# Optimization experiments

Hardware: AMD Instinct MI355X
Metric: run time of the kernel (lower is better)

The kernel has to match this reference:

```python
import jax, jax.numpy as jnp
import numpy as np

IN_SIZE = 224
KERNEL = 5
STRIDE = 1
IN_CH = 16
OUT_CH = 64
LAMB = 5.0
LR = 0.005
GAMMA = 0.99
EPS_ = 0.01
NH = (IN_SIZE - KERNEL) // STRIDE + 1          # 220 output positions per side
NB_TILES = NH * NH                              # 48400 tiles


def setup_inputs() -> dict:
    key = jax.random.key(0)
    k1, k2 = jax.random.split(key)
    x = jax.random.normal(k1, (1, IN_CH, IN_SIZE, IN_SIZE), dtype=jnp.float32)
    # torch.nn.init.uniform_(param, a=0, b=1)
    W = jax.random.uniform(k2, (OUT_CH, IN_CH, KERNEL, KERNEL), dtype=jnp.float32)
    exp_avg = jnp.zeros((OUT_CH,), dtype=jnp.float32)
    return {"x": x, "W": W, "exp_avg": exp_avg, "clamped": 0}


def _inhibition(out):
    out = jax.nn.relu(out)
    m = jnp.max(out, axis=1, keepdims=True)     # max over channel dim
    out = out / (m + 1e-9)
    return out ** LAMB


def _flatten_input(x):
    # mirrors x.unfold(2,k,s).unfold(3,k,s) -> [T, C*k*k] with (C, kh, kw) ordering
    starts = jnp.arange(NH) * STRIDE
    rows = starts[:, None] + jnp.arange(KERNEL)  # [NH, K]
    p = x[0][:, rows]                            # [C, NH, K, W]
    p = p[:, :, :, rows]                         # [C, NH, K, NH, K]
    p = p.transpose(1, 3, 0, 2, 4)               # [NH, NH, C, K, K]
    return p.reshape(NB_TILES, -1)               # [T, D]


def reference(x, W, exp_avg, clamped):
    # forward conv + inhibition
    out = jax.lax.conv_general_dilated(
        x, W, (STRIDE, STRIDE), 'VALID',
        dimension_numbers=('NCHW', 'OIHW', 'NCHW'))
    out = _inhibition(out)                       # [1, O, NH, NH]

    # Hebbian FullyOrthogonal update (no-grad buffer update in the original)
    y = out[0].transpose(1, 2, 0).reshape(-1, OUT_CH)   # [T, O]
    xf = _flatten_input(x)                               # [T, D]
    Wf = W.reshape(OUT_CH, -1)                           # [O, D]
    # mean_t( lr * (y_t (x) x_t - y_t (x) (y_t W)) ) = lr/T * (Y^T X - (Y^T Y) W)
    yty = y.T @ y                                        # [O, O]
    avg_delta = (LR / NB_TILES) * (y.T @ xf - yty @ Wf)  # [O, D]
    Wnew = jax.nn.relu(Wf + avg_delta).reshape(OUT_CH, IN_CH, KERNEL, KERNEL)
    exp_new = GAMMA * exp_avg + (1.0 - GAMMA) * jnp.mean(y, axis=0)

    # weight decay scaling
    A = exp_new / jnp.mean(exp_new)
    gfp = EPS_ * jnp.tanh(-EPS_ * (A - 1.0)) + 1.0
    gfn = 1.0 / gfp
    pos = jnp.where(Wnew > 0, Wnew, 0.0) * gfp.reshape(-1, 1, 1, 1)
    neg = jnp.where(Wnew < 0, Wnew, 0.0) * gfn.reshape(-1, 1, 1, 1)
    Wfinal = pos + neg
    return out, Wfinal, exp_new
```

## Files before the change

kernel.cpp:

```cpp
#include <hip/hip_runtime.h>
#include <stdint.h>

#define IN_SIZE 224
#define KER 5
#define IN_CH 16
#define OUT_CH 64
#define NH 220
#define NB_TILES (NH * NH)
#define XCH (IN_SIZE * IN_SIZE)
#define OUT_PLANE NB_TILES
#define KP2 51200
#define XS 52224
#define XTROWS 50304
#define LR_OVER_NB ((float)(0.005 / 48400.0))
#define GAMMA_F 0.99f
#define ONE_MINUS_GAMMA 0.01f
#define EPS_F 0.01f

#define NCHUNK 64
#define CK 800
#define PSTRIDE (64 * 512)
#define BROW 24

typedef __attribute__((ext_vector_type(8))) short short8;
typedef __attribute__((ext_vector_type(4))) float floatx4;

__device__ inline uint16_t f2bf(float f) {
    uint32_t u = __float_as_uint(f);
    return (uint16_t)((u + 0x7FFFu + ((u >> 16) & 1u)) >> 16);
}
__device__ inline float bf2f(uint16_t h) { return __uint_as_float((uint32_t)h << 16); }

__global__ __launch_bounds__(256) void prepa_kernel(const float* __restrict__ x,
                                                    uint16_t* __restrict__ xth,
                                                    uint16_t* __restrict__ xtl,
                                                    const float* __restrict__ W,
                                                    uint16_t* __restrict__ wrh,
                                                    uint16_t* __restrict__ wrl) {
    int blk = blockIdx.x;
    if (blk < 197) {
        int addr = blk * 256 + threadIdx.x;
        if (addr >= XTROWS) return;
        uint32_t dh[8], dl[8];
        if (addr < XCH) {
#pragma unroll
            for (int q = 0; q < 8; q++) {
                float v0 = x[(2 * q) * XCH + addr];
                float v1 = x[(2 * q + 1) * XCH + addr];
                uint16_t h0 = f2bf(v0), h1 = f2bf(v1);
                uint16_t l0 = f2bf(v0 - bf2f(h0)), l1 = f2bf(v1 - bf2f(h1));
                dh[q] = (uint32_t)h0 | ((uint32_t)h1 << 16);
                dl[q] = (uint32_t)l0 | ((uint32_t)l1 << 16);
            }
        } else {
#pragma unroll
            for (int q = 0; q < 8; q++) { dh[q] = 0u; dl[q] = 0u; }
        }
        *(uint4*)(xth + addr * 16) = make_uint4(dh[0], dh[1], dh[2], dh[3]);
        *(uint4*)(xth + addr * 16 + 8) = make_uint4(dh[4], dh[5], dh[6], dh[7]);
        *(uint4*)(xtl + addr * 16) = make_uint4(dl[0], dl[1], dl[2], dl[3]);
        *(uint4*)(xtl + addr * 16 + 8) = make_uint4(dl[4], dl[5], dl[6], dl[7]);
    } else {
        int idx = (blk - 197) * 256 + threadIdx.x;
        if (idx >= 13 * 4 * 64 * 8) return;
        int j = idx & 7;
        int lane = (idx >> 3) & 63;
        int ocg = (idx >> 9) & 3;
        int t = idx >> 11;
        int k = (lane >> 4) * 8 + j;
        int s = k >> 4, c = k & 15;
        int oc = 16 * ocg + (lane & 15);
        int tap = 2 * t + s;
        float v = (tap < 25) ? W[oc * 400 + c * 25 + tap] : 0.f;
        uint16_t h = f2bf(v);
        wrh[idx] = h;
        wrl[idx] = f2bf(v - bf2f(h));
    }
}

__global__ __launch_bounds__(256) void conv_prep_kernel(const uint16_t* __restrict__ xth,
                                                        const uint16_t* __restrict__ xtl,
                                                        const uint16_t* __restrict__ wrh,
                                                        const uint16_t* __restrict__ wrl,
                                                        float* __restrict__ out,
                                                        uint16_t* __restrict__ yb,
                                                        const float* __restrict__ x,
                                                        uint16_t* __restrict__ xs,
                                                        uint16_t* __restrict__ ones) {
    if (blockIdx.x >= 770) {
        int t = (blockIdx.x - 770) * 256 + threadIdx.x;
        const int perq = XS / 4;
        if (t < 5 * 16 * perq) {
            int kj = t / (16 * perq);
            int rem = t - kj * (16 * perq);
            int c = rem / perq;
            int q = (rem - c * perq) * 4;
            int base = c * XCH;
            ushort4 o;
            int i0 = q + kj;     o.x = f2bf(x[base + (i0 < XCH ? i0 : XCH - 1)]);
            int i1 = q + kj + 1; o.y = f2bf(x[base + (i1 < XCH ? i1 : XCH - 1)]);
            int i2 = q + kj + 2; o.z = f2bf(x[base + (i2 < XCH ? i2 : XCH - 1)]);
            int i3 = q + kj + 3; o.w = f2bf(x[base + (i3 < XCH ? i3 : XCH - 1)]);
            *(ushort4*)(xs + (kj * 16 + c) * XS + q) = o;
        }
        ushort4 z = {0, 0, 0, 0};
        if (t < 64 * 480) {
            int r = t / 480, q = (t - r * 480) * 4;
            *(ushort4*)(yb + r * KP2 + 49280 + q) = z;
        }
        if (t < 64 * 220) {
            int o = t / 220, i = t - o * 220;
            *(ushort4*)(yb + o * KP2 + i * 224 + 220) = z;
        }
        if (t < 12816) {
            ushort4 o1 = {0x3F80, 0x3F80, 0x3F80, 0x3F80};
            ((ushort4*)ones)[t] = o1;
        }
        return;
    }

    const int lane = threadIdx.x & 63;
    const int w = threadIdx.x >> 6;
    const int l15 = lane & 15;
    const int quad = lane >> 4;
    const int P0 = blockIdx.x * 64;
    const int c0 = (quad & 1) * 8;
    const int sq = quad >> 1;

    __shared__ uint16_t bsh[5 * 68 * BROW];
    __shared__ uint16_t bsl[5 * 68 * BROW];
    for (int u = threadIdx.x; u < 680; u += 256) {
        int row = u >> 1;
        int half = (u & 1) * 8;
        int strip = row / 68;
        int rr = row - strip * 68;
        int grow = P0 + strip * 224 + rr;
        *(uint4*)(bsh + row * BROW + half) = *(const uint4*)(xth + grow * 16 + half);
        *(uint4*)(bsl + row * BROW + half) = *(const uint4*)(xtl + grow * 16 + half);
    }
    __syncthreads();

    floatx4 acc[4];
#pragma unroll
    for (int g = 0; g < 4; g++) acc[g] = (floatx4){0.f, 0.f, 0.f, 0.f};

#pragma unroll
    for (int t = 0; t < 13; t++) {
        short8 ah = *(const short8*)(wrh + ((t * 4 + w) * 64 + lane) * 8);
        short8 al = *(const short8*)(wrl + ((t * 4 + w) * 64 + lane) * 8);
        const int tap0 = 2 * t, tap1 = 2 * t + 1;
        const int ki0 = tap0 / 5, kj0 = tap0 % 5;
        const int ki1 = (tap1 <= 24) ? tap1 / 5 : 0;
        const int kj1 = (tap1 <= 24) ? tap1 % 5 : 0;
        const int strip = sq ? ki1 : ki0;
        const int kjv = sq ? kj1 : kj0;
#pragma unroll
        for (int g = 0; g < 4; g++) {
            int lrow = strip * 68 + 16 * g + l15 + kjv;
            short8 bh = *(const short8*)(bsh + lrow * BROW + c0);
            short8 bl = *(const short8*)(bsl + lrow * BROW + c0);
            acc[g] = __builtin_amdgcn_mfma_f32_16x16x32_bf16(ah, bh, acc[g], 0, 0, 0);
            acc[g] = __builtin_amdgcn_mfma_f32_16x16x32_bf16(ah, bl, acc[g], 0, 0, 0);
            acc[g] = __builtin_amdgcn_mfma_f32_16x16x32_bf16(al, bh, acc[g], 0, 0, 0);
        }
    }

    __shared__ float wmax[4][64];
    float pmax[4];
#pragma unroll
    for (int g = 0; g < 4; g++) {
        float mx = fmaxf(fmaxf(acc[g][0], acc[g][1]), fmaxf(acc[g][2], acc[g][3]));
        mx = fmaxf(mx, 0.f);
        mx = fmaxf(mx, __shfl_xor(mx, 16));
        mx = fmaxf(mx, __shfl_xor(mx, 32));
        pmax[g] = mx;
    }
    if (quad == 0) {
#pragma unroll
        for (int g = 0; g < 4; g++) wmax[w][g * 16 + l15] = pmax[g];
    }
    __syncthreads();

#pragma unroll
    for (int g = 0; g < 4; g++) {
        int P = P0 + 16 * g + l15;
        int i = P / 224;
        int j = P - i * 224;
        bool valid = j < NH;
        float mx = fmaxf(fmaxf(wmax[0][g * 16 + l15], wmax[1][g * 16 + l15]),
                         fmaxf(wmax[2][g * 16 + l15], wmax[3][g * 16 + l15]));
        float inv = 1.f / (mx + 1e-9f);
#pragma unroll
        for (int r = 0; r < 4; r++) {
            float tv = fmaxf(acc[g][r], 0.f) * inv;
            float t2 = tv * tv;
            tv = t2 * t2 * tv;
            if (valid) {
                int oc = 16 * w + quad * 4 + r;
                out[oc * OUT_PLANE + i * NH + j] = tv;
                yb[oc * KP2 + P] = f2bf(tv);
            }
        }
    }
}

__global__ __launch_bounds__(256) void gemm_kernel(const uint16_t* __restrict__ yb,
                                                   const uint16_t* __restrict__ xs,
                                                   const uint16_t* __restrict__ ones,
                                                   float* __restrict__ Mpart) {
    __shared__ uint16_t As[2][64 * 40];
    __shared__ uint16_t Bs[2][64 * 40];
    const int tid = threadIdx.x;
    const int lane = tid & 63;
    const int w = tid >> 6;
    const int l15 = lane & 15;
    const int quad = lane >> 4;
    const int kg = quad * 8;
    const int b = blockIdx.x;
    const int xcd = b & 7;
    const int t8 = b >> 3;
    const int ntile = t8 & 7;
    const int chunk = xcd + 8 * (t8 >> 3);
    const int k0 = chunk * CK;

    const int sr = tid >> 2;
    const int sseg = (tid & 3) * 8;
    const uint16_t* pa = yb + sr * KP2 + k0 + sseg;

    int n_g = ntile * 64 + sr;
    const uint16_t* pbase;
    if (n_g < 400) {
        int c = n_g / 25;
        int r = n_g - 25 * c;
        int ki = r / 5;
        int kj = r - 5 * ki;
        pbase = xs + (kj * 16 + c) * XS + ki * 224;
    } else if (n_g < 464) {
        pbase = yb + (n_g - 400) * KP2;
    } else if (n_g == 464) {
        pbase = ones;
    } else {
        pbase = yb;
    }
    const uint16_t* pb = pbase + k0 + sseg;

    floatx4 acc[4];
#pragma unroll
    for (int i = 0; i < 4; i++) acc[i] = (floatx4){0.f, 0.f, 0.f, 0.f};

    uint4 ra = *(const uint4*)pa;
    uint4 rb = *(const uint4*)pb;

    for (int s = 0; s < 25; s++) {
        const int p = s & 1;
        *(uint4*)&As[p][sr * 40 + sseg] = ra;
        *(uint4*)&Bs[p][sr * 40 + sseg] = rb;
        __syncthreads();
        if (s + 1 < 25) {
            pa += 32;
            pb += 32;
            ra = *(const uint4*)pa;
            rb = *(const uint4*)pb;
        }
        short8 af = *(const short8*)&As[p][(16 * w + l15) * 40 + kg];
#pragma unroll
        for (int ng = 0; ng < 4; ng++) {
            short8 bf = *(const short8*)&Bs[p][(16 * ng + l15) * 40 + kg];
            acc[ng] = __builtin_amdgcn_mfma_f32_16x16x32_bf16(af, bf, acc[ng], 0, 0, 0);
        }
    }

    float* dst = Mpart + chunk * PSTRIDE;
#pragma unroll
    for (int ng = 0; ng < 4; ng++) {
        int col = ntile * 64 + ng * 16 + l15;
        if (col < 465) {
#pragma unroll
            for (int r = 0; r < 4; r++)
                dst[(16 * w + quad * 4 + r) * 512 + col] = acc[ng][r];
        }
    }
}

__global__ __launch_bounds__(256) void finalize_w_kernel(const float* __restrict__ W,
                                                         const float* __restrict__ Mpart,
                                                         const float* __restrict__ exp_avg,
                                                         float* __restrict__ Wout,
                                                         float* __restrict__ expout) {
    __shared__ float gfps[OUT_CH];
    __shared__ float ytys[2][OUT_CH];
    const int tid = threadIdx.x;
    const int bid = blockIdx.x;
    const int first_o = (bid * 256) / 400;

    if (tid < OUT_CH) {
        int o = tid;
        float cs = 0.f;
#pragma unroll 8
        for (int ch = 0; ch < NCHUNK; ch++) cs += Mpart[ch * PSTRIDE + o * 512 + 464];
        float e = GAMMA_F * exp_avg[o] + ONE_MINUS_GAMMA * (cs / (float)NB_TILES);
        float s = e;
        for (int off = 32; off; off >>= 1) s += __shfl_down(s, off);
        s = __shfl(s, 0);
        float A = e / (s / (float)OUT_CH);
        gfps[o] = EPS_F * tanhf(-EPS_F * (A - 1.f)) + 1.f;
        if (bid == 0) expout[o] = e;
    }
    if (tid >= 128) {
        int t = tid - 128;
        int orow = first_o + (t >> 6);
        int k = t & 63;
        float s = 0.f;
        if (orow < OUT_CH) {
#pragma unroll 8
            for (int ch = 0; ch < NCHUNK; ch++) s += Mpart[ch * PSTRIDE + orow * 512 + 400 + k];
        }
        ytys[t >> 6][k] = s;
    }
    __syncthreads();

    int idx = bid * 256 + tid;
    int o = idx / 400;
    int q = idx - o * 400;
    float Mv = 0.f;
#pragma unroll 8
    for (int ch = 0; ch < NCHUNK; ch++) Mv += Mpart[ch * PSTRIDE + o * 512 + q];
    const float* yrow = ytys[o - first_o];
    float dot = 0.f;
#pragma unroll 8
    for (int k = 0; k < OUT_CH; k++) dot = fmaf(yrow[k], W[k * 400 + q], dot);
    float wv = W[idx] + LR_OVER_NB * (Mv - dot);
    wv = fmaxf(wv, 0.f);
    float gp = gfps[o];
    float pos = (wv > 0.f ? wv : 0.f) * gp;
    float neg = (wv < 0.f ? wv : 0.f) / gp;
    Wout[idx] = pos + neg;
}

extern "C" void kernel_launch(void* const* d_in, const int* in_sizes, int n_in,
                              void* d_out, int out_size, void* d_ws, size_t ws_size,
                              hipStream_t stream) {
    const float* x = (const float*)d_in[0];
    const float* W = (const float*)d_in[1];
    const float* exp_avg = (const float*)d_in[2];
    float* out = (float*)d_out;

    float* wsf = (float*)d_ws;
    float* Mpart = wsf + 29760;
    uint16_t* xth = (uint16_t*)Mpart;
    uint16_t* xtl = xth + XTROWS * 16;
    uint16_t* wrh = xtl + XTROWS * 16;
    uint16_t* wrl = wrh + 26624;
    uint16_t* ybf = (uint16_t*)(wsf + 29760 + NCHUNK * PSTRIDE);
    uint16_t* xsb = ybf + OUT_CH * KP2;
    uint16_t* ones = xsb + 5 * 16 * XS;

    float* Wout = out + OUT_CH * OUT_PLANE;
    float* expout = Wout + OUT_CH * IN_CH * KER * KER;

    prepa_kernel<<<301, 256, 0, stream>>>(x, xth, xtl, W, wrh, wrl);
    conv_prep_kernel<<<770 + 4080, 256, 0, stream>>>(xth, xtl, wrh, wrl, out, ybf, x, xsb, ones);
    gemm_kernel<<<512, 256, 0, stream>>>(ybf, xsb, ones, Mpart);
    finalize_w_kernel<<<100, 256, 0, stream>>>(W, Mpart, exp_avg, Wout, expout);
}
```

Measured before the change: 110.3 us.

## Feed GEMM from fp32 conv output directly and store partial sums in bf16

Drops the separate padded bf16 copy of the inhibited activations (yb) and its zero-fill pass. The GEMM kernel now reads the fp32 conv output directly, handling row padding in a small loader, and converts to bf16 while staging into shared memory. The per-chunk partial-sum buffer is also stored as bf16 rather than fp32, halving its write and read traffic in finalize. The cost is twice the bytes per A/B activation load in the GEMM, plus reduced accuracy in the 64 partial sums that are accumulated into the weight update.

```diff
diff --git a/kernel.cpp b/kernel.cpp
--- a/kernel.cpp
+++ b/kernel.cpp
@@ -9,7 +9,7 @@
 #define NB_TILES (NH * NH)
 #define XCH (IN_SIZE * IN_SIZE)
 #define OUT_PLANE NB_TILES
-#define KP2 51200
+#define KPAD 49280
 #define XS 52224
 #define XTROWS 50304
 #define LR_OVER_NB ((float)(0.005 / 48400.0))
@@ -30,6 +30,31 @@
     return (uint16_t)((u + 0x7FFFu + ((u >> 16) & 1u)) >> 16);
 }
 __device__ inline float bf2f(uint16_t h) { return __uint_as_float((uint32_t)h << 16); }
+
+__device__ inline void load8f(const float* __restrict__ rowbase, int k, float* v) {
+    if (k >= KPAD) {
+#pragma unroll
+        for (int t = 0; t < 8; t++) v[t] = 0.f;
+        return;
+    }
+    int i = k / 224;
+    int j0 = k - i * 224;
+    const float* p = rowbase + i * NH + j0;
+    if (j0 <= 208) {
+        *(float4*)v = *(const float4*)p;
+        *(float4*)(v + 4) = *(const float4*)(p + 4);
+    } else {
+        *(float4*)v = *(const float4*)p;
+        v[4] = 0.f; v[5] = 0.f; v[6] = 0.f; v[7] = 0.f;
+    }
+}
+__device__ inline uint4 pack8(const float* v) {
+    uint32_t d[4];
+#pragma unroll
+    for (int t = 0; t < 4; t++)
+        d[t] = (uint32_t)f2bf(v[2 * t]) | ((uint32_t)f2bf(v[2 * t + 1]) << 16);
+    return *(uint4*)d;
+}
 
 __global__ __launch_bounds__(256) void prepa_kernel(const float* __restrict__ x,
                                                     uint16_t* __restrict__ xth,
@@ -83,7 +108,6 @@
                                                         const uint16_t* __restrict__ wrh,
                                                         const uint16_t* __restrict__ wrl,
                                                         float* __restrict__ out,
-                                                        uint16_t* __restrict__ yb,
                                                         const float* __restrict__ x,
                                                         uint16_t* __restrict__ xs,
                                                         uint16_t* __restrict__ ones) {
@@ -103,15 +127,6 @@
             int i3 = q + kj + 3; o.w = f2bf(x[base + (i3 < XCH ? i3 : XCH - 1)]);
             *(ushort4*)(xs + (kj * 16 + c) * XS + q) = o;
         }
-        ushort4 z = {0, 0, 0, 0};
-        if (t < 64 * 480) {
-            int r = t / 480, q = (t - r * 480) * 4;
-            *(ushort4*)(yb + r * KP2 + 49280 + q) = z;
-        }
-        if (t < 64 * 220) {
-            int o = t / 220, i = t - o * 220;
-            *(ushort4*)(yb + o * KP2 + i * 224 + 220) = z;
-        }
         if (t < 12816) {
             ushort4 o1 = {0x3F80, 0x3F80, 0x3F80, 0x3F80};
             ((ushort4*)ones)[t] = o1;
@@ -198,16 +213,15 @@
             if (valid) {
                 int oc = 16 * w + quad * 4 + r;
                 out[oc * OUT_PLANE + i * NH + j] = tv;
-                yb[oc * KP2 + P] = f2bf(tv);
             }
         }
     }
 }
 
-__global__ __launch_bounds__(256) void gemm_kernel(const uint16_t* __restrict__ yb,
+__global__ __launch_bounds__(256) void gemm_kernel(const float* __restrict__ out,
                                                    const uint16_t* __restrict__ xs,
                                                    const uint16_t* __restrict__ ones,
-                                                   float* __restrict__ Mpart) {
+                                                   uint16_t* __restrict__ Mpart) {
     __shared__ uint16_t As[2][64 * 40];
     __shared__ uint16_t Bs[2][64 * 40];
     const int tid = threadIdx.x;
@@ -225,42 +239,43 @@
 
     const int sr = tid >> 2;
     const int sseg = (tid & 3) * 8;
-    const uint16_t* pa = yb + sr * KP2 + k0 + sseg;
+    const float* aof = out + sr * OUT_PLANE;
+    int ka = k0 + sseg;
 
     int n_g = ntile * 64 + sr;
-    const uint16_t* pbase;
+    bool b_out = (n_g >= 400 && n_g < 464);
+    const float* bof = b_out ? out + (n_g - 400) * OUT_PLANE : out;
+    const uint16_t* pb;
     if (n_g < 400) {
         int c = n_g / 25;
         int r = n_g - 25 * c;
         int ki = r / 5;
         int kj = r - 5 * ki;
-        pbase = xs + (kj * 16 + c) * XS + ki * 224;
-    } else if (n_g < 464) {
-        pbase = yb + (n_g - 400) * KP2;
-    } else if (n_g == 464) {
-        pbase = ones;
+        pb = xs + (kj * 16 + c) * XS + ki * 224 + k0 + sseg;
     } else {
-        pbase = yb;
-    }
-    const uint16_t* pb = pbase + k0 + sseg;
+        pb = ones + k0 + sseg;
+    }
 
     floatx4 acc[4];
 #pragma unroll
     for (int i = 0; i < 4; i++) acc[i] = (floatx4){0.f, 0.f, 0.f, 0.f};
 
-    uint4 ra = *(const uint4*)pa;
-    uint4 rb = *(const uint4*)pb;
+    float av[8], bv[8];
+    uint4 rbd;
+    load8f(aof, ka, av);
+    if (b_out) load8f(bof, ka, bv);
+    else rbd = *(const uint4*)pb;
 
     for (int s = 0; s < 25; s++) {
         const int p = s & 1;
-        *(uint4*)&As[p][sr * 40 + sseg] = ra;
-        *(uint4*)&Bs[p][sr * 40 + sseg] = rb;
+        *(uint4*)&As[p][sr * 40 + sseg] = pack8(av);
+        *(uint4*)&Bs[p][sr * 40 + sseg] = b_out ? pack8(bv) : rbd;
         __syncthreads();
         if (s + 1 < 25) {
-            pa += 32;
-            pb += 32;
-            ra = *(const uint4*)pa;
-            rb = *(const uint4*)pb;
+            ka += 32;
+            load8f(aof, ka, av);
+            if (b_out) load8f(bof, ka, bv);
+            else { pb += 32; rbd = *(const uint4*)pb; }
         }
         short8 af = *(const short8*)&As[p][(16 * w + l15) * 40 + kg];
 #pragma unroll
@@ -270,20 +285,20 @@
         }
     }
 
-    float* dst = Mpart + chunk * PSTRIDE;
+    uint16_t* dst = Mpart + chunk * PSTRIDE;
 #pragma unroll
     for (int ng = 0; ng < 4; ng++) {
         int col = ntile * 64 + ng * 16 + l15;
         if (col < 465) {
 #pragma unroll
             for (int r = 0; r < 4; r++)
-                dst[(16 * w + quad * 4 + r) * 512 + col] = acc[ng][r];
+                dst[(16 * w + quad * 4 + r) * 512 + col] = f2bf(acc[ng][r]);
         }
     }
 }
 
 __global__ __launch_bounds__(256) void finalize_w_kernel(const float* __restrict__ W,
-                                                         const float* __restrict__ Mpart,
+                                                         const uint16_t* __restrict__ Mpart,
                                                          const float* __restrict__ exp_avg,
                                                          float* __restrict__ Wout,
                                                          float* __restrict__ expout) {
@@ -297,7 +312,7 @@
         int o = tid;
         float cs = 0.f;
 #pragma unroll 8
-        for (int ch = 0; ch < NCHUNK; ch++) cs += Mpart[ch * PSTRIDE + o * 512 + 464];
+        for (int ch = 0; ch < NCHUNK; ch++) cs += bf2f(Mpart[ch * PSTRIDE + o * 512 + 464]);
         float e = GAMMA_F * exp_avg[o] + ONE_MINUS_GAMMA * (cs / (float)NB_TILES);
         float s = e;
         for (int off = 32; off; off >>= 1) s += __shfl_down(s, off);
@@ -313,7 +328,7 @@
         float s = 0.f;
         if (orow < OUT_CH) {
 #pragma unroll 8
-            for (int ch = 0; ch < NCHUNK; ch++) s += Mpart[ch * PSTRIDE + orow * 512 + 400 + k];
+            for (int ch = 0; ch < NCHUNK; ch++) s += bf2f(Mpart[ch * PSTRIDE + orow * 512 + 400 + k]);
         }
         ytys[t >> 6][k] = s;
     }
@@ -324,7 +339,7 @@
     int q = idx - o * 400;
     float Mv = 0.f;
 #pragma unroll 8
-    for (int ch = 0; ch < NCHUNK; ch++) Mv += Mpart[ch * PSTRIDE + o * 512 + q];
+    for (int ch = 0; ch < NCHUNK; ch++) Mv += bf2f(Mpart[ch * PSTRIDE + o * 512 + q]);
     const float* yrow = ytys[o - first_o];
     float dot = 0.f;
 #pragma unroll 8
@@ -345,21 +360,19 @@
     const float* exp_avg = (const float*)d_in[2];
     float* out = (float*)d_out;
 
-    float* wsf = (float*)d_ws;
-    float* Mpart = wsf + 29760;
-    uint16_t* xth = (uint16_t*)Mpart;
+    uint16_t* Mpart = (uint16_t*)d_ws;
+    uint16_t* xth = Mpart;
     uint16_t* xtl = xth + XTROWS * 16;
     uint16_t* wrh = xtl + XTROWS * 16;
     uint16_t* wrl = wrh + 26624;
-    uint16_t* ybf = (uint16_t*)(wsf + 29760 + NCHUNK * PSTRIDE);
-    uint16_t* xsb = ybf + OUT_CH * KP2;
+    uint16_t* xsb = Mpart + NCHUNK * PSTRIDE;
     uint16_t* ones = xsb + 5 * 16 * XS;
 
     float* Wout = out + OUT_CH * OUT_PLANE;
     float* expout = Wout + OUT_CH * IN_CH * KER * KER;
 
     prepa_kernel<<<301, 256, 0, stream>>>(x, xth, xtl, W, wrh, wrl);
-    conv_prep_kernel<<<770 + 4080, 256, 0, stream>>>(xth, xtl, wrh, wrl, out, ybf, x, xsb, ones);
-    gemm_kernel<<<512, 256, 0, stream>>>(ybf, xsb, ones, Mpart);
+    conv_prep_kernel<<<770 + 4080, 256, 0, stream>>>(xth, xtl, wrh, wrl, out, x, xsb, ones);
+    gemm_kernel<<<512, 256, 0, stream>>>(out, xsb, ones, Mpart);
     finalize_w_kernel<<<100, 256, 0, stream>>>(W, Mpart, exp_avg, Wout, expout);
 }
```

Result: slower. 117.6 us (+6.6%).
